# Kernel tuning notes

Hardware: AMD Instinct MI355X
Metric: run time of the kernel (lower is better)

Reference implementation:

```python
import jax, jax.numpy as jnp
import numpy as np
from jax import lax

TEMP = 20.0    # args.temp
ATT_WT = 0.5   # args.att_wt
EPS = 1e-12


def l2norm(x, axis):
    # torch F.normalize: x / max(||x||_2, eps)
    n = jnp.sqrt(jnp.sum(x * x, axis=axis, keepdims=True))
    return x / jnp.maximum(n, EPS)


def conv4d(x, w):
    """4D conv, padding=1, stride=1.
    x: [B,Cin,H1,W1,H2,W2], w: [Cout,Cin,3,3,3,3] -> [B,Cout,H1,W1,H2,W2].
    Decomposed as 9 fixed (di,dj) shifts over (H1,W1), each a 2D conv over (H2,W2).
    """
    B, Cin, H1, W1, H2, W2 = x.shape
    Cout = w.shape[0]
    xp = jnp.pad(x, ((0, 0), (0, 0), (1, 1), (1, 1), (0, 0), (0, 0)))
    out = jnp.zeros((B * H1 * W1, Cout, H2, W2), x.dtype)
    for di in range(3):
        for dj in range(3):
            xs = xp[:, :, di:di + H1, dj:dj + W1]                      # [B,Cin,H1,W1,H2,W2]
            xr = xs.transpose(0, 2, 3, 1, 4, 5).reshape(B * H1 * W1, Cin, H2, W2)
            out = out + lax.conv_general_dilated(
                xr, w[:, :, di, dj], (1, 1), 'SAME',
                dimension_numbers=('NCHW', 'OIHW', 'NCHW'))
    return out.reshape(B, H1, W1, Cout, H2, W2).transpose(0, 3, 1, 2, 4, 5)


def nc_stack(x, ws):
    for w in ws:
        x = jax.nn.relu(conv4d(x, w))
    return x


def neigh_consensus(corr, ws):
    # symmetric mode: conv(C) + perm(conv(perm(C)))
    ct = corr.transpose(0, 1, 4, 5, 2, 3)
    return nc_stack(corr, ws) + nc_stack(ct, ws).transpose(0, 1, 4, 5, 2, 3)


def setup_inputs() -> dict:
    key = jax.random.key(0)
    ks = jax.random.split(key, 7)
    L, B, C, h, w = 9, 2, 1024, 20, 20
    ch = 256
    return {
        'fq_feats': jax.random.normal(ks[0], (L, B, C, h, w), jnp.float32),
        'fs_feats': jax.random.normal(ks[1], (L, B, C, h, w), jnp.float32),
        'f_q': jax.random.normal(ks[2], (B, ch, h, w), jnp.float32),
        'f_s': jax.random.normal(ks[3], (B, ch, h, w), jnp.float32),
        'w1': jax.random.normal(ks[4], (10, 9, 3, 3, 3, 3), jnp.float32) * 0.1,
        'w2': jax.random.normal(ks[5], (10, 10, 3, 3, 3, 3), jnp.float32) * 0.1,
        'w3': jax.random.normal(ks[6], (1, 10, 3, 3, 3, 3), jnp.float32) * 0.1,
    }


def reference(fq_feats, fs_feats, f_q, f_s, w1, w2, w3):
    L, B, C, h, w = fq_feats.shape
    ch = f_q.shape[1]
    hw = h * w
    # per-level channel-wise L2 normalization -> cosine correlation volume
    fqn = l2norm(fq_feats, axis=2)
    fsn = l2norm(fs_feats, axis=2)
    # corr4d[b,l,i,j,k,m] = <fq[:, i,j], fs[:, k,m]>  -> [B, L, h, w, h, w]
    corr4d = jnp.einsum('lbcij,lbckm->blijkm', fqn, fsn)
    # neighbourhood-consensus matching net -> [B,1,h,w,h,w]
    c4 = neigh_consensus(corr4d, (w1, w2, w3))
    attn = jax.nn.softmax(c4.reshape(B, hw, hw) * TEMP, axis=-1)  # over support positions
    v = f_s.reshape(B, ch, hw)
    att_fq = jnp.einsum('bqs,bcs->bcq', attn, v).reshape(B, ch, h, w)
    fq = l2norm(f_q, axis=1) + l2norm(att_fq, axis=1) * ATT_WT
    return (fq, att_fq)
```

## Files before the change

### kernel.cpp

```cpp
#include <hip/hip_runtime.h>
#include <math.h>
#include <stddef.h>

#define L9   9
#define NB   2
#define CF   1024
#define HW   400
#define CH   256
#define TEMPF 20.0f
#define EPSF  1e-12f

typedef _Float16 half8 __attribute__((ext_vector_type(8)));
typedef float f32x4 __attribute__((ext_vector_type(4)));
typedef unsigned short ushort_t;

__global__ __launch_bounds__(256) void norm_partial2(const float* __restrict__ fq,
                                                     const float* __restrict__ fs,
                                                     float* __restrict__ partial2) {
    int chunk = blockIdx.x, lb = blockIdx.y, t = blockIdx.z;
    int tid = threadIdx.x;
    if (tid >= 200) return;
    int half = tid / 100, p4 = tid - half * 100;
    const float* src = (t == 0 ? fq : fs) + (size_t)lb * CF * HW + p4 * 4;
    int c0 = chunk * 64 + half;
    f32x4 acc = {};
    #pragma unroll 8
    for (int it = 0; it < 32; ++it) {
        const float4 v = *(const float4*)(src + (size_t)(c0 + it * 2) * HW);
        acc[0] = fmaf(v.x, v.x, acc[0]);
        acc[1] = fmaf(v.y, v.y, acc[1]);
        acc[2] = fmaf(v.z, v.z, acc[2]);
        acc[3] = fmaf(v.w, v.w, acc[3]);
    }
    float* dst = partial2 + ((size_t)((t * 18 + lb) * 32) + chunk * 2 + half) * HW + p4 * 4;
    *(f32x4*)dst = acc;
}

__global__ __launch_bounds__(256) void norm_finalize2(const float* __restrict__ partial2,
                                                      float* __restrict__ invn) {
    int idx = blockIdx.x * 256 + threadIdx.x;
    if (idx >= 2 * 18 * HW) return;
    int t_lb = idx / HW;
    int ij = idx - t_lb * HW;
    const float* p = partial2 + (size_t)t_lb * 32 * HW + ij;
    float ss = 0.f;
    #pragma unroll
    for (int c = 0; c < 32; ++c) ss += p[c * HW];
    invn[idx] = 1.0f / fmaxf(sqrtf(ss), EPSF);
}

__global__ __launch_bounds__(256) void transpose_f16(const float* __restrict__ fq,
                                                     const float* __restrict__ fs,
                                                     ushort_t* __restrict__ At,
                                                     ushort_t* __restrict__ Bt,
                                                     int lb_base) {
    __shared__ float tile[64][65];
    int z = blockIdx.z;
    int tsel = z / 9, li = z - tsel * 9;
    int lb = lb_base + li;
    const float* src = (tsel ? fs : fq) + (size_t)lb * CF * HW;
    ushort_t* dst = (tsel ? Bt : At) + (size_t)li * HW * CF;
    int c0 = blockIdx.x * 64, ij0 = blockIdx.y * 64;
    int tid = threadIdx.x;
    int cl = tid >> 6;
    int col = tid & 63;
    #pragma unroll
    for (int rr = 0; rr < 16; ++rr) {
        int c_local = rr * 4 + cl;
        int ij = ij0 + col;
        tile[c_local][col] = (ij < HW) ? src[(size_t)(c0 + c_local) * HW + ij] : 0.f;
    }
    __syncthreads();
    int cp = (tid & 31) * 2;
    int rowsel = tid >> 5;
    #pragma unroll
    for (int rr = 0; rr < 8; ++rr) {
        int ij_local = rr * 8 + rowsel;
        int ij = ij0 + ij_local;
        if (ij < HW) {
            union { _Float16 h; ushort_t u; } h0, h1;
            h0.h = (_Float16)tile[cp][ij_local];
            h1.h = (_Float16)tile[cp + 1][ij_local];
            ushort2 o; o.x = h0.u; o.y = h1.u;
            *(ushort2*)(dst + (size_t)ij * CF + c0 + cp) = o;
        }
    }
}

__global__ __launch_bounds__(256) void corr_gemm_mfma(const ushort_t* __restrict__ At,
                                                      const ushort_t* __restrict__ Bt,
                                                      const float* __restrict__ invn,
                                                      ushort_t* __restrict__ corr,
                                                      int lb_base) {
    __shared__ ushort_t As[64][72];
    __shared__ ushort_t Bs[64][72];
    int li = blockIdx.z, lb = lb_base + li;
    int l = lb >> 1, b = lb & 1;
    int i0 = blockIdx.y * 64, j0 = blockIdx.x * 64;
    int tid = threadIdx.x, lane = tid & 63, w = tid >> 6;
    int mw = (w >> 1) * 32, nw = (w & 1) * 32;
    f32x4 acc[2][2] = {};
    const ushort_t* Abase = At + (size_t)li * HW * CF;
    const ushort_t* Bbase = Bt + (size_t)li * HW * CF;

    for (int kt = 0; kt < 16; ++kt) {
        int c0 = kt * 64;
        __syncthreads();
        #pragma unroll
        for (int p = 0; p < 2; ++p) {
            int idx = tid + p * 256;
            int row = idx >> 3, c8 = idx & 7;
            uint4 va = make_uint4(0, 0, 0, 0), vb = make_uint4(0, 0, 0, 0);
            if (i0 + row < HW) va = *(const uint4*)(Abase + (size_t)(i0 + row) * CF + c0 + c8 * 8);
            if (j0 + row < HW) vb = *(const uint4*)(Bbase + (size_t)(j0 + row) * CF + c0 + c8 * 8);
            *(uint4*)&As[row][c8 * 8] = va;
            *(uint4*)&Bs[row][c8 * 8] = vb;
        }
        __syncthreads();
        #pragma unroll
        for (int ks = 0; ks < 2; ++ks) {
            int k0 = ks * 32 + (lane >> 4) * 8;
            half8 a0 = *(const half8*)&As[mw + (lane & 15)][k0];
            half8 a1 = *(const half8*)&As[mw + 16 + (lane & 15)][k0];
            half8 b0 = *(const half8*)&Bs[nw + (lane & 15)][k0];
            half8 b1 = *(const half8*)&Bs[nw + 16 + (lane & 15)][k0];
            acc[0][0] = __builtin_amdgcn_mfma_f32_16x16x32_f16(a0, b0, acc[0][0], 0, 0, 0);
            acc[0][1] = __builtin_amdgcn_mfma_f32_16x16x32_f16(a0, b1, acc[0][1], 0, 0, 0);
            acc[1][0] = __builtin_amdgcn_mfma_f32_16x16x32_f16(a1, b0, acc[1][0], 0, 0, 0);
            acc[1][1] = __builtin_amdgcn_mfma_f32_16x16x32_f16(a1, b1, acc[1][1], 0, 0, 0);
        }
    }
    int obase = (b * 9 + l) * HW;
    #pragma unroll
    for (int mi = 0; mi < 2; ++mi) {
        #pragma unroll
        for (int ni = 0; ni < 2; ++ni) {
            #pragma unroll
            for (int r = 0; r < 4; ++r) {
                int ij = i0 + mw + mi * 16 + (lane >> 4) * 4 + r;
                int km = j0 + nw + ni * 16 + (lane & 15);
                if (ij < HW && km < HW) {
                    union { _Float16 h; ushort_t u; } cv;
                    cv.h = (_Float16)(acc[mi][ni][r] * invn[lb * HW + ij] * invn[7200 + lb * HW + km]);
                    corr[(size_t)(obase + ij) * HW + km] = cv.u;
                }
            }
        }
    }
}

template <int CIN, int COUT, bool SWAP>
__global__ __launch_bounds__(256) void wprep7(const float* __restrict__ wt,
                                              ushort_t* __restrict__ wb) {
    constexpr int S = CIN * 9;
    constexpr int NCH = (S + 31) / 32;
    int idx = blockIdx.x * 256 + threadIdx.x;
    int total = NCH * 4608;
    if (idx >= total) return;
    int k = idx & 31, n = (idx >> 5) & 15, dd = (idx >> 9) % 9, ch = idx / 4608;
    int slot = ch * 32 + k;
    float v = 0.f;
    if (n < COUT && slot < S) {
        int ci = slot / 9, pl = slot - ci * 9;
        int di = pl / 3, dj = pl % 3, dk = dd / 3, dm = dd % 3;
        int widx = SWAP ? ((((n * CIN + ci) * 3 + dk) * 3 + dm) * 3 + di) * 3 + dj
                        : ((((n * CIN + ci) * 3 + di) * 3 + dj) * 3 + dk) * 3 + dm;
        v = wt[widx];
    }
    union { _Float16 h; ushort_t u; } cv; cv.h = (_Float16)v;
    wb[idx] = cv.u;
}

template <int CIN, int COUT, bool SWAP, int MODE>
__global__ __launch_bounds__(256) void wprep12(const float* __restrict__ wt,
                                               ushort_t* __restrict__ wb) {
    constexpr int S2 = CIN * 12;
    constexpr int NCH = (S2 + 31) / 32;
    int idx = blockIdx.x * 256 + threadIdx.x;
    int total = NCH * 4608;
    if (idx >= total) return;
    int k = idx & 31, n = (idx >> 5) & 15, dd = (idx >> 9) % 9, ch = idx / 4608;
    int slot = ch * 32 + k;
    float v = 0.f;
    if (slot < S2) {
        int ci = slot / 12, r = slot - ci * 12;
        int di = r >> 2, dj4 = r & 3;
        int dk = dd / 3, dm = dd % 3;
        int off = (MODE == 2) ? n : MODE;
        int e = dj4 - off;
        int nn = (MODE == 2) ? 0 : n;
        bool ok = (MODE == 2) ? (n < 2) : (n < COUT);
        if (ok && e >= 0 && e <= 2) {
            int widx = SWAP ? ((((nn * CIN + ci) * 3 + dk) * 3 + dm) * 3 + di) * 3 + e
                            : ((((nn * CIN + ci) * 3 + di) * 3 + e) * 3 + dk) * 3 + dm;
            v = wt[widx];
        }
    }
    union { _Float16 h; ushort_t u; } cv; cv.h = (_Float16)v;
    wb[idx] = cv.u;
}

template <int CIN, int COUT>
__global__ __launch_bounds__(256) void conv4d_l1(const ushort_t* __restrict__ in,
                                                 const ushort_t* __restrict__ wbA,
                                                 const ushort_t* __restrict__ wbB,
                                                 ushort_t* __restrict__ outA,
                                                 ushort_t* __restrict__ outB) {
    constexpr int S = CIN * 9;
    constexpr int NCH = (S + 31) / 32;
    __shared__ __align__(16) ushort_t Ah[484 * 40];
    const int b = blockIdx.y, ij = blockIdx.x;
    const int i = ij / 20, j = ij - (ij / 20) * 20;
    const int tid = threadIdx.x, wv = tid >> 6, lane = tid & 63;
    const int m16 = lane & 15, q4 = lane >> 4;

    for (int p = tid; p < 484 * 20; p += 256) ((uint*)Ah)[p] = 0;

    int baseh[7];
    #pragma unroll
    for (int s = 0; s < 7; ++s) {
        int t = wv + 4 * s;
        if (t < 25) {
            int km = t * 16 + m16;
            int kk = km / 20, mm = km - kk * 20;
            baseh[s] = (kk * 22 + mm) * 40 + q4 * 8;
        } else baseh[s] = 0;
    }
    f32x4 accA[7] = {};
    f32x4 accB[7] = {};

    const bool stager = tid < 200;
    const int km1 = 2 * tid;
    const int r1 = stager ? ((km1 / 20 + 1) * 22 + (km1 % 20) + 1) : 0;
    int hofs[9]; bool vld[9];
    #pragma unroll
    for (int pl = 0; pl < 9; ++pl) {
        int ii = i + pl / 3 - 1, jj = j + pl % 3 - 1;
        vld[pl] = (unsigned)ii < 20u && (unsigned)jj < 20u;
        hofs[pl] = (ii * 20 + jj) * HW + km1;
    }
    const ushort_t* in_b = in + (size_t)b * CIN * HW * HW;
    const int wbase = m16 * 32 + q4 * 8;

    uint pf[32];
    #pragma unroll
    for (int u = 0; u < 32; ++u) {
        int slot = u;
        if (slot < S) {
            int ci = slot / 9, pl = slot - ci * 9;
            pf[u] = (stager && vld[pl]) ? *(const uint*)(in_b + ci * (HW * HW) + hofs[pl]) : 0u;
        } else pf[u] = 0u;
    }
    __syncthreads();

    #pragma unroll
    for (int ch = 0; ch < NCH; ++ch) {
        if (stager) {
            #pragma unroll
            for (int g4 = 0; g4 < 8; ++g4) {
                uint lo0 = (pf[4 * g4] & 0xFFFFu) | (pf[4 * g4 + 1] << 16);
                uint lo1 = (pf[4 * g4 + 2] & 0xFFFFu) | (pf[4 * g4 + 3] << 16);
                uint hi0 = (pf[4 * g4] >> 16) | (pf[4 * g4 + 1] & 0xFFFF0000u);
                uint hi1 = (pf[4 * g4 + 2] >> 16) | (pf[4 * g4 + 3] & 0xFFFF0000u);
                uint2 wlo; wlo.x = lo0; wlo.y = lo1;
                uint2 whi; whi.x = hi0; whi.y = hi1;
                *(uint2*)&Ah[(size_t)r1 * 40 + 4 * g4] = wlo;
                *(uint2*)&Ah[(size_t)(r1 + 1) * 40 + 4 * g4] = whi;
            }
        }
        __syncthreads();
        if (ch + 1 < NCH) {
            #pragma unroll
            for (int u = 0; u < 32; ++u) {
                int slot = (ch + 1) * 32 + u;
                if (slot < S) {
                    int ci = slot / 9, pl = slot - ci * 9;
                    pf[u] = (stager && vld[pl]) ? *(const uint*)(in_b + ci * (HW * HW) + hofs[pl]) : 0u;
                } else pf[u] = 0u;
            }
        }
        #pragma unroll
        for (int dd = 0; dd < 9; ++dd) {
            half8 bfA = *(const half8*)(wbA + (ch * 9 + dd) * 512 + wbase);
            half8 bfB = *(const half8*)(wbB + (ch * 9 + dd) * 512 + wbase);
            const int doff = ((dd / 3) * 22 + (dd % 3)) * 40;
            #pragma unroll
            for (int s = 0; s < 7; ++s) {
                if (wv + 4 * s < 25) {
                    half8 af = *(const half8*)(Ah + baseh[s] + doff);
                    accA[s] = __builtin_amdgcn_mfma_f32_16x16x32_f16(af, bfA, accA[s], 0, 0, 0);
                    accB[s] = __builtin_amdgcn_mfma_f32_16x16x32_f16(af, bfB, accB[s], 0, 0, 0);
                }
            }
        }
        if (ch + 1 < NCH) __syncthreads();
    }

    const int co = m16;
    if (co < COUT) {
        #pragma unroll
        for (int s = 0; s < 7; ++s) {
            int t = wv + 4 * s;
            if (t < 25) {
                int km0 = t * 16 + q4 * 4;
                size_t o = ((size_t)(b * COUT + co) * HW + ij) * HW + km0;
                union { ushort_t us[4]; uint2 u2; } pk;
                #pragma unroll
                for (int r = 0; r < 4; ++r) {
                    union { _Float16 h; ushort_t u16; } cv;
                    cv.h = (_Float16)fmaxf(accA[s][r], 0.f);
                    pk.us[r] = cv.u16;
                }
                *(uint2*)(outA + o) = pk.u2;
                #pragma unroll
                for (int r = 0; r < 4; ++r) {
                    union { _Float16 h; ushort_t u16; } cv;
                    cv.h = (_Float16)fmaxf(accB[s][r], 0.f);
                    pk.us[r] = cv.u16;
                }
                *(uint2*)(outB + o) = pk.u2;
            }
        }
    }
}

template <int CIN, int COUT, bool MERGED, bool OUTF16>
__global__ __launch_bounds__(256) void conv4d_2ij(
        const ushort_t* __restrict__ inA, const ushort_t* __restrict__ inB,
        const ushort_t* __restrict__ wA1, const ushort_t* __restrict__ wA2,
        const ushort_t* __restrict__ wB1, const ushort_t* __restrict__ wB2,
        void* __restrict__ outA, void* __restrict__ outB) {
    constexpr int S2 = CIN * 12;
    constexpr int NCH = (S2 + 31) / 32;
    __shared__ __align__(16) ushort_t Ah[484 * 40];
    const int b = blockIdx.y, bx = blockIdx.x, z = blockIdx.z;
    const ushort_t* in = z ? inB : inA;
    const ushort_t* w1 = z ? wB1 : wA1;
    const ushort_t* w2 = z ? wB2 : wA2;
    void* outS = z ? outB : outA;
    const int i = bx / 10, jp = bx - (bx / 10) * 10;
    const int j0 = 2 * jp;
    const int ij0 = i * 20 + j0;
    const int tid = threadIdx.x, wv = tid >> 6, lane = tid & 63;
    const int m16 = lane & 15, q4 = lane >> 4;

    for (int p = tid; p < 484 * 20; p += 256) ((uint*)Ah)[p] = 0;

    int baseh[7];
    #pragma unroll
    for (int s = 0; s < 7; ++s) {
        int t = wv + 4 * s;
        if (t < 25) {
            int km = t * 16 + m16;
            int kk = km / 20, mm = km - kk * 20;
            baseh[s] = (kk * 22 + mm) * 40 + q4 * 8;
        } else baseh[s] = 0;
    }
    f32x4 acc1[7] = {};
    f32x4 acc2[7] = {};

    const bool stager = tid < 200;
    const int km1 = 2 * tid;
    const int r1 = stager ? ((km1 / 20 + 1) * 22 + (km1 % 20) + 1) : 0;
    int hofs[12]; bool vld[12];
    #pragma unroll
    for (int pl = 0; pl < 12; ++pl) {
        int di = pl >> 2, dj = pl & 3;
        int ii = i + di - 1, jj = j0 + dj - 1;
        vld[pl] = (unsigned)ii < 20u && (unsigned)jj < 20u;
        hofs[pl] = (ii * 20 + jj) * HW + km1;
    }
    const ushort_t* in_b = in + (size_t)b * CIN * HW * HW;
    const int wbase = m16 * 32 + q4 * 8;

    uint pf[32];
    #pragma unroll
    for (int u = 0; u < 32; ++u) {
        int slot = u;
        if (slot < S2) {
            int ci = slot / 12, pl = slot - ci * 12;
            pf[u] = (stager && vld[pl]) ? *(const uint*)(in_b + ci * (HW * HW) + hofs[pl]) : 0u;
        } else pf[u] = 0u;
    }
    __syncthreads();

    #pragma unroll
    for (int ch = 0; ch < NCH; ++ch) {
        if (stager) {
            #pragma unroll
            for (int g4 = 0; g4 < 8; ++g4) {
                uint lo0 = (pf[4 * g4] & 0xFFFFu) | (pf[4 * g4 + 1] << 16);
                uint lo1 = (pf[4 * g4 + 2] & 0xFFFFu) | (pf[4 * g4 + 3] << 16);
                uint hi0 = (pf[4 * g4] >> 16) | (pf[4 * g4 + 1] & 0xFFFF0000u);
                uint hi1 = (pf[4 * g4 + 2] >> 16) | (pf[4 * g4 + 3] & 0xFFFF0000u);
                uint2 wlo; wlo.x = lo0; wlo.y = lo1;
                uint2 whi; whi.x = hi0; whi.y = hi1;
                *(uint2*)&Ah[(size_t)r1 * 40 + 4 * g4] = wlo;
                *(uint2*)&Ah[(size_t)(r1 + 1) * 40 + 4 * g4] = whi;
            }
        }
        __syncthreads();
        if (ch + 1 < NCH) {
            #pragma unroll
            for (int u = 0; u < 32; ++u) {
                int slot = (ch + 1) * 32 + u;
                if (slot < S2) {
                    int ci = slot / 12, pl = slot - ci * 12;
                    pf[u] = (stager && vld[pl]) ? *(const uint*)(in_b + ci * (HW * HW) + hofs[pl]) : 0u;
                } else pf[u] = 0u;
            }
        }
        #pragma unroll
        for (int dd = 0; dd < 9; ++dd) {
            half8 bf1 = *(const half8*)(w1 + (ch * 9 + dd) * 512 + wbase);
            half8 bf2;
            if (!MERGED) bf2 = *(const half8*)(w2 + (ch * 9 + dd) * 512 + wbase);
            const int doff = ((dd / 3) * 22 + (dd % 3)) * 40;
            #pragma unroll
            for (int s = 0; s < 7; ++s) {
                if (wv + 4 * s < 25) {
                    half8 af = *(const half8*)(Ah + baseh[s] + doff);
                    acc1[s] = __builtin_amdgcn_mfma_f32_16x16x32_f16(af, bf1, acc1[s], 0, 0, 0);
                    if (!MERGED) acc2[s] = __builtin_amdgcn_mfma_f32_16x16x32_f16(af, bf2, acc2[s], 0, 0, 0);
                }
            }
        }
        if (ch + 1 < NCH) __syncthreads();
    }

    if (MERGED) {
        if (m16 < 2) {
            const int ij = ij0 + m16;
            #pragma unroll
            for (int s = 0; s < 7; ++s) {
                int t = wv + 4 * s;
                if (t < 25) {
                    int km0 = t * 16 + q4 * 4;
                    size_t o = ((size_t)b * HW + ij) * HW + km0;
                    f32x4 ov;
                    #pragma unroll
                    for (int r = 0; r < 4; ++r) ov[r] = fmaxf(acc1[s][r], 0.f);
                    *(f32x4*)((float*)outS + o) = ov;
                }
            }
        }
    } else {
        const int co = m16;
        if (co < COUT) {
            #pragma unroll
            for (int s = 0; s < 7; ++s) {
                int t = wv + 4 * s;
                if (t < 25) {
                    int km0 = t * 16 + q4 * 4;
                    size_t o = ((size_t)(b * COUT + co) * HW + ij0) * HW + km0;
                    if (OUTF16) {
                        union { ushort_t us[4]; uint2 u2; } pk;
                        #pragma unroll
                        for (int r = 0; r < 4; ++r) {
                            union { _Float16 h; ushort_t u16; } cv;
                            cv.h = (_Float16)fmaxf(acc1[s][r], 0.f);
                            pk.us[r] = cv.u16;
                        }
                        *(uint2*)((ushort_t*)outS + o) = pk.u2;
                        #pragma unroll
                        for (int r = 0; r < 4; ++r) {
                            union { _Float16 h; ushort_t u16; } cv;
                            cv.h = (_Float16)fmaxf(acc2[s][r], 0.f);
                            pk.us[r] = cv.u16;
                        }
                        *(uint2*)((ushort_t*)outS + o + HW) = pk.u2;
                    } else {
                        f32x4 ov;
                        #pragma unroll
                        for (int r = 0; r < 4; ++r) ov[r] = fmaxf(acc1[s][r], 0.f);
                        *(f32x4*)((float*)outS + o) = ov;
                        #pragma unroll
                        for (int r = 0; r < 4; ++r) ov[r] = fmaxf(acc2[s][r], 0.f);
                        *(f32x4*)((float*)outS + o + HW) = ov;
                    }
                }
            }
        }
    }
}

__global__ __launch_bounds__(256) void fs_prep(const float* __restrict__ f_s,
                                               ushort_t* __restrict__ fsh) {
    int idx = blockIdx.x * 256 + threadIdx.x;
    if (idx >= NB * CH * 416) return;
    int s = idx % 416, bc = idx / 416;
    float v = (s < HW) ? f_s[(size_t)bc * HW + s] : 0.f;
    union { _Float16 h; ushort_t u; } cv; cv.h = (_Float16)v;
    fsh[idx] = cv.u;
}

__global__ __launch_bounds__(256) void softmax_av_mfma2(const float* __restrict__ c4A,
                                                        const float* __restrict__ c4B,
                                                        const ushort_t* __restrict__ fsh,
                                                        float* __restrict__ att) {
    __shared__ ushort_t P[64 * 424];
    __shared__ float invl[64];
    const int b = blockIdx.z, qb = blockIdx.x * 64;
    const int tid = threadIdx.x, wv = tid >> 6, lane = tid & 63;
    const int m16 = lane & 15, q4 = lane >> 4;
    const int lane16 = lane & 15, rg4 = lane >> 4;

    #pragma unroll 1
    for (int rg = 0; rg < 4; ++rg) {
        const int ql = wv * 16 + rg * 4 + rg4;
        int q = qb + ql; if (q > HW - 1) q = HW - 1;
        const float* rowA = c4A + ((size_t)b * HW + q) * HW;
        const float* rowB = c4B + ((size_t)b * HW + q) * HW;
        float4 v4[7];
        #pragma unroll
        for (int k4 = 0; k4 < 6; ++k4) {
            float4 a4 = *(const float4*)(rowA + 64 * k4 + lane16 * 4);
            float4 b4 = *(const float4*)(rowB + 64 * k4 + lane16 * 4);
            v4[k4] = make_float4(a4.x + b4.x, a4.y + b4.y, a4.z + b4.z, a4.w + b4.w);
        }
        if (lane16 < 4) {
            float4 a4 = *(const float4*)(rowA + 384 + lane16 * 4);
            float4 b4 = *(const float4*)(rowB + 384 + lane16 * 4);
            v4[6] = make_float4(a4.x + b4.x, a4.y + b4.y, a4.z + b4.z, a4.w + b4.w);
        } else {
            v4[6] = make_float4(-1e30f, -1e30f, -1e30f, -1e30f);
        }
        float mx = -1e30f;
        #pragma unroll
        for (int k4 = 0; k4 < 7; ++k4)
            mx = fmaxf(mx, fmaxf(fmaxf(v4[k4].x, v4[k4].y), fmaxf(v4[k4].z, v4[k4].w)));
        #pragma unroll
        for (int off = 8; off; off >>= 1) mx = fmaxf(mx, __shfl_xor(mx, off, 16));
        float sum = 0.f;
        #pragma unroll
        for (int k4 = 0; k4 < 7; ++k4) {
            if (k4 == 6 && lane16 >= 4) break;
            float e0 = __expf(TEMPF * (v4[k4].x - mx));
            float e1 = __expf(TEMPF * (v4[k4].y - mx));
            float e2 = __expf(TEMPF * (v4[k4].z - mx));
            float e3 = __expf(TEMPF * (v4[k4].w - mx));
            sum += e0 + e1 + e2 + e3;
            union { ushort_t us[4]; uint2 u2; } pk;
            union { _Float16 h; ushort_t u16; } cv;
            cv.h = (_Float16)e0; pk.us[0] = cv.u16;
            cv.h = (_Float16)e1; pk.us[1] = cv.u16;
            cv.h = (_Float16)e2; pk.us[2] = cv.u16;
            cv.h = (_Float16)e3; pk.us[3] = cv.u16;
            *(uint2*)&P[(size_t)ql * 424 + 64 * k4 + lane16 * 4] = pk.u2;
        }
        if (lane16 >= 4 && lane16 < 10) {
            uint2 z2; z2.x = 0; z2.y = 0;
            *(uint2*)&P[(size_t)ql * 424 + 384 + lane16 * 4] = z2;
        }
        #pragma unroll
        for (int off = 8; off; off >>= 1) sum += __shfl_xor(sum, off, 16);
        if (lane16 == 0) invl[ql] = 1.0f / sum;
    }

    half8 afr[13];
    #pragma unroll
    for (int ks = 0; ks < 13; ++ks)
        afr[ks] = *(const half8*)&P[(size_t)(wv * 16 + m16) * 424 + ks * 32 + q4 * 8];
    const ushort_t* fb = fsh + (size_t)b * CH * 416;
    #pragma unroll
    for (int ntl = 0; ntl < 2; ++ntl) {
        const int nt = blockIdx.y * 2 + ntl;
        const int c = nt * 16 + m16;
        const ushort_t* fc = fb + (size_t)c * 416 + q4 * 8;
        f32x4 acc = {};
        #pragma unroll
        for (int ks = 0; ks < 13; ++ks) {
            half8 bf = *(const half8*)(fc + ks * 32);
            acc = __builtin_amdgcn_mfma_f32_16x16x32_f16(afr[ks], bf, acc, 0, 0, 0);
        }
        #pragma unroll
        for (int r = 0; r < 4; ++r) {
            int ql = wv * 16 + q4 * 4 + r;
            int q = qb + ql;
            if (q < HW)
                att[((size_t)b * CH + c) * HW + q] = acc[r] * invl[ql];
        }
    }
}

__global__ __launch_bounds__(256) void final_fq(const float* __restrict__ f_q,
                                                const float* __restrict__ att,
                                                float* __restrict__ out_fq) {
    __shared__ float red[256];
    int b = blockIdx.y, q = blockIdx.x;
    int tid = threadIdx.x;
    size_t idx = (size_t)(b * CH + tid) * HW + q;
    float f = f_q[idx];
    float a = att[idx];
    red[tid] = f * f;
    __syncthreads();
    for (int s = 128; s > 0; s >>= 1) {
        if (tid < s) red[tid] += red[tid + s];
        __syncthreads();
    }
    float invf = 1.0f / fmaxf(sqrtf(red[0]), EPSF);
    __syncthreads();
    red[tid] = a * a;
    __syncthreads();
    for (int s = 128; s > 0; s >>= 1) {
        if (tid < s) red[tid] += red[tid + s];
        __syncthreads();
    }
    float inva = 1.0f / fmaxf(sqrtf(red[0]), EPSF);
    out_fq[idx] = f * invf + 0.5f * a * inva;
}

extern "C" void kernel_launch(void* const* d_in, const int* in_sizes, int n_in,
                              void* d_out, int out_size, void* d_ws, size_t ws_size,
                              hipStream_t stream) {
    const float* fq_feats = (const float*)d_in[0];
    const float* fs_feats = (const float*)d_in[1];
    const float* f_q      = (const float*)d_in[2];
    const float* f_s      = (const float*)d_in[3];
    const float* w1       = (const float*)d_in[4];
    const float* w2       = (const float*)d_in[5];
    const float* w3       = (const float*)d_in[6];
    float* out = (float*)d_out;

    float* ws      = (float*)d_ws;
    float* wbuf    = ws;
    float* invn    = wbuf + 115200;
    float* corr    = invn + 14400;
    float* buf1    = corr + 2880000;
    float* buf2    = buf1 + 3200000;
    float* att     = out + 204800;

    float* partial2 = buf1;
    ushort_t* corr_h = (ushort_t*)corr;
    ushort_t* fsh    = (ushort_t*)(corr + 1440000);
    float* c4A = corr + 1600000;
    float* c4B = corr + 1920000;
    ushort_t* At = (ushort_t*)buf1;
    ushort_t* Bt = (ushort_t*)buf2;
    ushort_t* b1A = (ushort_t*)buf1;
    ushort_t* b1B = b1A + 3200000;
    ushort_t* b2A = (ushort_t*)buf2;
    ushort_t* b2B = b2A + 3200000;

    ushort_t* wb0    = (ushort_t*)wbuf;
    ushort_t* wbL1A  = wb0;
    ushort_t* wbL1B  = wb0 + 13824;
    ushort_t* wbL2A0 = wb0 + 27648;
    ushort_t* wbL2A1 = wb0 + 46080;
    ushort_t* wbL2B0 = wb0 + 64512;
    ushort_t* wbL2B1 = wb0 + 82944;
    ushort_t* wbL3Am = wb0 + 101376;
    ushort_t* wbL3Bm = wb0 + 119808;

    norm_partial2<<<dim3(16, 18, 2), 256, 0, stream>>>(fq_feats, fs_feats, partial2);
    norm_finalize2<<<(2 * 18 * HW + 255) / 256, 256, 0, stream>>>(partial2, invn);

    wprep7<9, 10, false><<<54, 256, 0, stream>>>(w1, wbL1A);
    wprep7<9, 10, true ><<<54, 256, 0, stream>>>(w1, wbL1B);
    wprep12<10, 10, false, 0><<<72, 256, 0, stream>>>(w2, wbL2A0);
    wprep12<10, 10, false, 1><<<72, 256, 0, stream>>>(w2, wbL2A1);
    wprep12<10, 10, true,  0><<<72, 256, 0, stream>>>(w2, wbL2B0);
    wprep12<10, 10, true,  1><<<72, 256, 0, stream>>>(w2, wbL2B1);
    wprep12<10, 1, false, 2><<<72, 256, 0, stream>>>(w3, wbL3Am);
    wprep12<10, 1, true,  2><<<72, 256, 0, stream>>>(w3, wbL3Bm);
    fs_prep<<<(NB * CH * 416 + 255) / 256, 256, 0, stream>>>(f_s, fsh);

    for (int half = 0; half < 2; ++half) {
        int base = half * 9;
        transpose_f16<<<dim3(16, 7, 18), 256, 0, stream>>>(fq_feats, fs_feats, At, Bt, base);
        corr_gemm_mfma<<<dim3(7, 7, 9), 256, 0, stream>>>(At, Bt, invn, corr_h, base);
    }

    conv4d_l1<9, 10><<<dim3(400, NB, 1), 256, 0, stream>>>(
        corr_h, wbL1A, wbL1B, b1A, b1B);
    conv4d_2ij<10, 10, false, true><<<dim3(200, NB, 2), 256, 0, stream>>>(
        b1A, b1B, wbL2A0, wbL2A1, wbL2B0, wbL2B1, b2A, b2B);
    conv4d_2ij<10, 1, true, false><<<dim3(200, NB, 2), 256, 0, stream>>>(
        b2A, b2B, wbL3Am, wbL3Am, wbL3Bm, wbL3Bm, c4A, c4B);

    softmax_av_mfma2<<<dim3(7, 8, NB), 256, 0, stream>>>(c4A, c4B, fsh, att);
    final_fq<<<dim3(400, NB), 256, 0, stream>>>(f_q, att, out);

    (void)in_sizes; (void)n_in; (void)out_size; (void)ws_size;
}
```

Before: 364.4 us.

## Merge prep kernels, fuse norm into transpose, restructure layer-2 conv and final reduction

Replaces the eight weight-prep launches, the f_s conversion and the ssbuf clear with one prep_all kernel. Drops the separate two-pass norm kernels by accumulating squared sums in transpose_f16 with atomics and taking the inverse square root in the GEMM epilogue. Layer 2 now runs the single-ij 9-tap conv kernel with one weight set per z, replacing the 2-ij 12-slot variant. final_fq switches its tree reduction to wavefront shuffles. This saves launches and a pass over the features, but adds atomics and redoes the sqrt/division per output element.

```diff
diff --git a/kernel.cpp b/kernel.cpp
--- a/kernel.cpp
+++ b/kernel.cpp
@@ -14,47 +14,69 @@
 typedef float f32x4 __attribute__((ext_vector_type(4)));
 typedef unsigned short ushort_t;
 
-__global__ __launch_bounds__(256) void norm_partial2(const float* __restrict__ fq,
-                                                     const float* __restrict__ fs,
-                                                     float* __restrict__ partial2) {
-    int chunk = blockIdx.x, lb = blockIdx.y, t = blockIdx.z;
-    int tid = threadIdx.x;
-    if (tid >= 200) return;
-    int half = tid / 100, p4 = tid - half * 100;
-    const float* src = (t == 0 ? fq : fs) + (size_t)lb * CF * HW + p4 * 4;
-    int c0 = chunk * 64 + half;
-    f32x4 acc = {};
-    #pragma unroll 8
-    for (int it = 0; it < 32; ++it) {
-        const float4 v = *(const float4*)(src + (size_t)(c0 + it * 2) * HW);
-        acc[0] = fmaf(v.x, v.x, acc[0]);
-        acc[1] = fmaf(v.y, v.y, acc[1]);
-        acc[2] = fmaf(v.z, v.z, acc[2]);
-        acc[3] = fmaf(v.w, v.w, acc[3]);
-    }
-    float* dst = partial2 + ((size_t)((t * 18 + lb) * 32) + chunk * 2 + half) * HW + p4 * 4;
-    *(f32x4*)dst = acc;
-}
-
-__global__ __launch_bounds__(256) void norm_finalize2(const float* __restrict__ partial2,
-                                                      float* __restrict__ invn) {
-    int idx = blockIdx.x * 256 + threadIdx.x;
-    if (idx >= 2 * 18 * HW) return;
-    int t_lb = idx / HW;
-    int ij = idx - t_lb * HW;
-    const float* p = partial2 + (size_t)t_lb * 32 * HW + ij;
-    float ss = 0.f;
-    #pragma unroll
-    for (int c = 0; c < 32; ++c) ss += p[c * HW];
-    invn[idx] = 1.0f / fmaxf(sqrtf(ss), EPSF);
+__global__ __launch_bounds__(256) void prep_all(const float* __restrict__ w1,
+                                                const float* __restrict__ w2,
+                                                const float* __restrict__ w3,
+                                                const float* __restrict__ f_s,
+                                                ushort_t* __restrict__ wb0,
+                                                ushort_t* __restrict__ fsh,
+                                                float* __restrict__ ssbuf) {
+    int gid = blockIdx.x * 256 + threadIdx.x;
+    if (gid < NB * CH * 416) {
+        int s = gid % 416, bc = gid / 416;
+        float v = (s < HW) ? f_s[(size_t)bc * HW + s] : 0.f;
+        union { _Float16 h; ushort_t u; } cv; cv.h = (_Float16)v;
+        fsh[gid] = cv.u;
+    }
+    if (gid < 14400) ssbuf[gid] = 0.f;
+    if (gid < 6 * 18432) {
+        int job = gid / 18432, idx = gid - job * 18432;
+        int k = idx & 31, n = (idx >> 5) & 15, dd = (idx >> 9) % 9, ch = idx / 4608;
+        int dk = dd / 3, dm = dd % 3;
+        float v = 0.f;
+        if (job < 4) {
+            if (idx < 13824) {
+                int CIN = (job < 2) ? 9 : 10;
+                const float* wt = (job < 2) ? w1 : w2;
+                bool swap = job & 1;
+                int slot = ch * 32 + k;
+                if (n < 10 && slot < CIN * 9) {
+                    int ci = slot / 9, pl = slot - ci * 9;
+                    int di = pl / 3, dj = pl % 3;
+                    int widx = swap ? ((((n * CIN + ci) * 3 + dk) * 3 + dm) * 3 + di) * 3 + dj
+                                    : ((((n * CIN + ci) * 3 + di) * 3 + dj) * 3 + dk) * 3 + dm;
+                    v = wt[widx];
+                }
+                union { _Float16 h; ushort_t u; } cv; cv.h = (_Float16)v;
+                wb0[job * 13824 + idx] = cv.u;
+            }
+        } else {
+            bool swap = (job == 5);
+            int slot = ch * 32 + k;
+            if (slot < 120) {
+                int ci = slot / 12, r = slot - ci * 12;
+                int di = r >> 2, dj4 = r & 3;
+                int e = dj4 - n;
+                if (n < 2 && e >= 0 && e <= 2) {
+                    int widx = swap ? (((ci * 3 + dk) * 3 + dm) * 3 + di) * 3 + e
+                                    : (((ci * 3 + di) * 3 + e) * 3 + dk) * 3 + dm;
+                    v = w3[widx];
+                }
+            }
+            union { _Float16 h; ushort_t u; } cv; cv.h = (_Float16)v;
+            wb0[55296 + (job - 4) * 18432 + idx] = cv.u;
+        }
+    }
 }
 
 __global__ __launch_bounds__(256) void transpose_f16(const float* __restrict__ fq,
                                                      const float* __restrict__ fs,
                                                      ushort_t* __restrict__ At,
                                                      ushort_t* __restrict__ Bt,
+                                                     float* __restrict__ ssbuf,
                                                      int lb_base) {
     __shared__ float tile[64][65];
+    __shared__ float red4[4][64];
     int z = blockIdx.z;
     int tsel = z / 9, li = z - tsel * 9;
     int lb = lb_base + li;
@@ -64,13 +86,24 @@
     int tid = threadIdx.x;
     int cl = tid >> 6;
     int col = tid & 63;
+    float ssp = 0.f;
     #pragma unroll
     for (int rr = 0; rr < 16; ++rr) {
         int c_local = rr * 4 + cl;
         int ij = ij0 + col;
-        tile[c_local][col] = (ij < HW) ? src[(size_t)(c0 + c_local) * HW + ij] : 0.f;
-    }
+        float v = (ij < HW) ? src[(size_t)(c0 + c_local) * HW + ij] : 0.f;
+        tile[c_local][col] = v;
+        ssp = fmaf(v, v, ssp);
+    }
+    red4[cl][col] = ssp;
     __syncthreads();
+    if (cl == 0) {
+        int ij = ij0 + col;
+        if (ij < HW) {
+            float s4 = red4[0][col] + red4[1][col] + red4[2][col] + red4[3][col];
+            atomicAdd(&ssbuf[(size_t)(tsel * 18 + lb) * HW + ij], s4);
+        }
+    }
     int cp = (tid & 31) * 2;
     int rowsel = tid >> 5;
     #pragma unroll
@@ -89,7 +122,7 @@
 
 __global__ __launch_bounds__(256) void corr_gemm_mfma(const ushort_t* __restrict__ At,
                                                       const ushort_t* __restrict__ Bt,
-                                                      const float* __restrict__ invn,
+                                                      const float* __restrict__ ssbuf,
                                                       ushort_t* __restrict__ corr,
                                                       int lb_base) {
     __shared__ ushort_t As[64][72];
@@ -132,16 +165,19 @@
     }
     int obase = (b * 9 + l) * HW;
     #pragma unroll
-    for (int mi = 0; mi < 2; ++mi) {
-        #pragma unroll
-        for (int ni = 0; ni < 2; ++ni) {
+    for (int ni = 0; ni < 2; ++ni) {
+        int km = j0 + nw + ni * 16 + (lane & 15);
+        if (km >= HW) continue;
+        float ib = 1.0f / fmaxf(sqrtf(ssbuf[(size_t)(18 + lb) * HW + km]), EPSF);
+        #pragma unroll
+        for (int mi = 0; mi < 2; ++mi) {
             #pragma unroll
             for (int r = 0; r < 4; ++r) {
                 int ij = i0 + mw + mi * 16 + (lane >> 4) * 4 + r;
-                int km = j0 + nw + ni * 16 + (lane & 15);
-                if (ij < HW && km < HW) {
+                if (ij < HW) {
+                    float ia = 1.0f / fmaxf(sqrtf(ssbuf[(size_t)lb * HW + ij]), EPSF);
                     union { _Float16 h; ushort_t u; } cv;
-                    cv.h = (_Float16)(acc[mi][ni][r] * invn[lb * HW + ij] * invn[7200 + lb * HW + km]);
+                    cv.h = (_Float16)(acc[mi][ni][r] * ia * ib);
                     corr[(size_t)(obase + ij) * HW + km] = cv.u;
                 }
             }
@@ -149,67 +185,21 @@
     }
 }
 
-template <int CIN, int COUT, bool SWAP>
-__global__ __launch_bounds__(256) void wprep7(const float* __restrict__ wt,
-                                              ushort_t* __restrict__ wb) {
-    constexpr int S = CIN * 9;
-    constexpr int NCH = (S + 31) / 32;
-    int idx = blockIdx.x * 256 + threadIdx.x;
-    int total = NCH * 4608;
-    if (idx >= total) return;
-    int k = idx & 31, n = (idx >> 5) & 15, dd = (idx >> 9) % 9, ch = idx / 4608;
-    int slot = ch * 32 + k;
-    float v = 0.f;
-    if (n < COUT && slot < S) {
-        int ci = slot / 9, pl = slot - ci * 9;
-        int di = pl / 3, dj = pl % 3, dk = dd / 3, dm = dd % 3;
-        int widx = SWAP ? ((((n * CIN + ci) * 3 + dk) * 3 + dm) * 3 + di) * 3 + dj
-                        : ((((n * CIN + ci) * 3 + di) * 3 + dj) * 3 + dk) * 3 + dm;
-        v = wt[widx];
-    }
-    union { _Float16 h; ushort_t u; } cv; cv.h = (_Float16)v;
-    wb[idx] = cv.u;
-}
-
-template <int CIN, int COUT, bool SWAP, int MODE>
-__global__ __launch_bounds__(256) void wprep12(const float* __restrict__ wt,
-                                               ushort_t* __restrict__ wb) {
-    constexpr int S2 = CIN * 12;
-    constexpr int NCH = (S2 + 31) / 32;
-    int idx = blockIdx.x * 256 + threadIdx.x;
-    int total = NCH * 4608;
-    if (idx >= total) return;
-    int k = idx & 31, n = (idx >> 5) & 15, dd = (idx >> 9) % 9, ch = idx / 4608;
-    int slot = ch * 32 + k;
-    float v = 0.f;
-    if (slot < S2) {
-        int ci = slot / 12, r = slot - ci * 12;
-        int di = r >> 2, dj4 = r & 3;
-        int dk = dd / 3, dm = dd % 3;
-        int off = (MODE == 2) ? n : MODE;
-        int e = dj4 - off;
-        int nn = (MODE == 2) ? 0 : n;
-        bool ok = (MODE == 2) ? (n < 2) : (n < COUT);
-        if (ok && e >= 0 && e <= 2) {
-            int widx = SWAP ? ((((nn * CIN + ci) * 3 + dk) * 3 + dm) * 3 + di) * 3 + e
-                            : ((((nn * CIN + ci) * 3 + di) * 3 + e) * 3 + dk) * 3 + dm;
-            v = wt[widx];
-        }
-    }
-    union { _Float16 h; ushort_t u; } cv; cv.h = (_Float16)v;
-    wb[idx] = cv.u;
-}
-
-template <int CIN, int COUT>
-__global__ __launch_bounds__(256) void conv4d_l1(const ushort_t* __restrict__ in,
+template <int CIN, int COUT, bool DUAL, bool OUTF16>
+__global__ __launch_bounds__(256) void conv4d_v8(const ushort_t* __restrict__ inA,
+                                                 const ushort_t* __restrict__ inB,
                                                  const ushort_t* __restrict__ wbA,
                                                  const ushort_t* __restrict__ wbB,
-                                                 ushort_t* __restrict__ outA,
-                                                 ushort_t* __restrict__ outB) {
+                                                 void* __restrict__ outA,
+                                                 void* __restrict__ outB) {
     constexpr int S = CIN * 9;
     constexpr int NCH = (S + 31) / 32;
     __shared__ __align__(16) ushort_t Ah[484 * 40];
     const int b = blockIdx.y, ij = blockIdx.x;
+    const int z = blockIdx.z;
+    const ushort_t* in = (DUAL || z == 0) ? inA : inB;
+    const ushort_t* wbS = (DUAL || z == 0) ? wbA : wbB;
+    void* outS = (DUAL || z == 0) ? outA : outB;
     const int i = ij / 20, j = ij - (ij / 20) * 20;
     const int tid = threadIdx.x, wv = tid >> 6, lane = tid & 63;
     const int m16 = lane & 15, q4 = lane >> 4;
@@ -281,15 +271,16 @@
         }
         #pragma unroll
         for (int dd = 0; dd < 9; ++dd) {
-            half8 bfA = *(const half8*)(wbA + (ch * 9 + dd) * 512 + wbase);
-            half8 bfB = *(const half8*)(wbB + (ch * 9 + dd) * 512 + wbase);
+            half8 bfA = *(const half8*)(wbS + (ch * 9 + dd) * 512 + wbase);
+            half8 bfB;
+            if (DUAL) bfB = *(const half8*)(wbB + (ch * 9 + dd) * 512 + wbase);
             const int doff = ((dd / 3) * 22 + (dd % 3)) * 40;
             #pragma unroll
             for (int s = 0; s < 7; ++s) {
                 if (wv + 4 * s < 25) {
                     half8 af = *(const half8*)(Ah + baseh[s] + doff);
                     accA[s] = __builtin_amdgcn_mfma_f32_16x16x32_f16(af, bfA, accA[s], 0, 0, 0);
-                    accB[s] = __builtin_amdgcn_mfma_f32_16x16x32_f16(af, bfB, accB[s], 0, 0, 0);
+                    if (DUAL) accB[s] = __builtin_amdgcn_mfma_f32_16x16x32_f16(af, bfB, accB[s], 0, 0, 0);
                 }
             }
         }
@@ -304,40 +295,47 @@
             if (t < 25) {
                 int km0 = t * 16 + q4 * 4;
                 size_t o = ((size_t)(b * COUT + co) * HW + ij) * HW + km0;
-                union { ushort_t us[4]; uint2 u2; } pk;
-                #pragma unroll
-                for (int r = 0; r < 4; ++r) {
-                    union { _Float16 h; ushort_t u16; } cv;
-                    cv.h = (_Float16)fmaxf(accA[s][r], 0.f);
-                    pk.us[r] = cv.u16;
+                if (OUTF16) {
+                    union { ushort_t us[4]; uint2 u2; } pk;
+                    #pragma unroll
+                    for (int r = 0; r < 4; ++r) {
+                        union { _Float16 h; ushort_t u16; } cv;
+                        cv.h = (_Float16)fmaxf(accA[s][r], 0.f);
+                        pk.us[r] = cv.u16;
+                    }
+                    *(uint2*)((ushort_t*)outS + o) = pk.u2;
+                    if (DUAL) {
+                        #pragma unroll
+                        for (int r = 0; r < 4; ++r) {
+                            union { _Float16 h; ushort_t u16; } cv;
+                            cv.h = (_Float16)fmaxf(accB[s][r], 0.f);
+                            pk.us[r] = cv.u16;
+                        }
+                        *(uint2*)((ushort_t*)outB + o) = pk.u2;
+                    }
+                } else {
+                    f32x4 ov;
+                    #pragma unroll
+                    for (int r = 0; r < 4; ++r) ov[r] = fmaxf(accA[s][r], 0.f);
+                    *(f32x4*)((float*)outS + o) = ov;
                 }
-                *(uint2*)(outA + o) = pk.u2;
-                #pragma unroll
-                for (int r = 0; r < 4; ++r) {
-                    union { _Float16 h; ushort_t u16; } cv;
-                    cv.h = (_Float16)fmaxf(accB[s][r], 0.f);
-                    pk.us[r] = cv.u16;
-                }
-                *(uint2*)(outB + o) = pk.u2;
-            }
-        }
-    }
-}
-
-template <int CIN, int COUT, bool MERGED, bool OUTF16>
-__global__ __launch_bounds__(256) void conv4d_2ij(
+            }
+        }
+    }
+}
+
+template <int CIN>
+__global__ __launch_bounds__(256) void conv4d_l3(
         const ushort_t* __restrict__ inA, const ushort_t* __restrict__ inB,
-        const ushort_t* __restrict__ wA1, const ushort_t* __restrict__ wA2,
-        const ushort_t* __restrict__ wB1, const ushort_t* __restrict__ wB2,
-        void* __restrict__ outA, void* __restrict__ outB) {
+        const ushort_t* __restrict__ wAm, const ushort_t* __restrict__ wBm,
+        float* __restrict__ outA, float* __restrict__ outB) {
     constexpr int S2 = CIN * 12;
     constexpr int NCH = (S2 + 31) / 32;
     __shared__ __align__(16) ushort_t Ah[484 * 40];
     const int b = blockIdx.y, bx = blockIdx.x, z = blockIdx.z;
     const ushort_t* in = z ? inB : inA;
-    const ushort_t* w1 = z ? wB1 : wA1;
-    const ushort_t* w2 = z ? wB2 : wA2;
-    void* outS = z ? outB : outA;
+    const ushort_t* w1 = z ? wBm : wAm;
+    float* outS = z ? outB : outA;
     const int i = bx / 10, jp = bx - (bx / 10) * 10;
     const int j0 = 2 * jp;
     const int ij0 = i * 20 + j0;
@@ -357,7 +355,6 @@
         } else baseh[s] = 0;
     }
     f32x4 acc1[7] = {};
-    f32x4 acc2[7] = {};
 
     const bool stager = tid < 200;
     const int km1 = 2 * tid;
@@ -413,85 +410,33 @@
         #pragma unroll
         for (int dd = 0; dd < 9; ++dd) {
             half8 bf1 = *(const half8*)(w1 + (ch * 9 + dd) * 512 + wbase);
-            half8 bf2;
-            if (!MERGED) bf2 = *(const half8*)(w2 + (ch * 9 + dd) * 512 + wbase);
             const int doff = ((dd / 3) * 22 + (dd % 3)) * 40;
             #pragma unroll
             for (int s = 0; s < 7; ++s) {
                 if (wv + 4 * s < 25) {
                     half8 af = *(const half8*)(Ah + baseh[s] + doff);
                     acc1[s] = __builtin_amdgcn_mfma_f32_16x16x32_f16(af, bf1, acc1[s], 0, 0, 0);
-                    if (!MERGED) acc2[s] = __builtin_amdgcn_mfma_f32_16x16x32_f16(af, bf2, acc2[s], 0, 0, 0);
                 }
             }
         }
         if (ch + 1 < NCH) __syncthreads();
     }
 
-    if (MERGED) {
-        if (m16 < 2) {
-            const int ij = ij0 + m16;
-            #pragma unroll
-            for (int s = 0; s < 7; ++s) {
-                int t = wv + 4 * s;
-                if (t < 25) {
-                    int km0 = t * 16 + q4 * 4;
-                    size_t o = ((size_t)b * HW + ij) * HW + km0;
-                    f32x4 ov;
-                    #pragma unroll
-                    for (int r = 0; r < 4; ++r) ov[r] = fmaxf(acc1[s][r], 0.f);
-                    *(f32x4*)((float*)outS + o) = ov;
-                }
-            }
-        }
-    } else {
-        const int co = m16;
-        if (co < COUT) {
-            #pragma unroll
-            for (int s = 0; s < 7; ++s) {
-                int t = wv + 4 * s;
-                if (t < 25) {
-                    int km0 = t * 16 + q4 * 4;
-                    size_t o = ((size_t)(b * COUT + co) * HW + ij0) * HW + km0;
-                    if (OUTF16) {
-                        union { ushort_t us[4]; uint2 u2; } pk;
-                        #pragma unroll
-                        for (int r = 0; r < 4; ++r) {
-                            union { _Float16 h; ushort_t u16; } cv;
-                            cv.h = (_Float16)fmaxf(acc1[s][r], 0.f);
-                            pk.us[r] = cv.u16;
-                        }
-                        *(uint2*)((ushort_t*)outS + o) = pk.u2;
-                        #pragma unroll
-                        for (int r = 0; r < 4; ++r) {
-                            union { _Float16 h; ushort_t u16; } cv;
-                            cv.h = (_Float16)fmaxf(acc2[s][r], 0.f);
-                            pk.us[r] = cv.u16;
-                        }
-                        *(uint2*)((ushort_t*)outS + o + HW) = pk.u2;
-                    } else {
-                        f32x4 ov;
-                        #pragma unroll
-                        for (int r = 0; r < 4; ++r) ov[r] = fmaxf(acc1[s][r], 0.f);
-                        *(f32x4*)((float*)outS + o) = ov;
-                        #pragma unroll
-                        for (int r = 0; r < 4; ++r) ov[r] = fmaxf(acc2[s][r], 0.f);
-                        *(f32x4*)((float*)outS + o + HW) = ov;
-                    }
-                }
-            }
-        }
-    }
-}
-
-__global__ __launch_bounds__(256) void fs_prep(const float* __restrict__ f_s,
-                                               ushort_t* __restrict__ fsh) {
-    int idx = blockIdx.x * 256 + threadIdx.x;
-    if (idx >= NB * CH * 416) return;
-    int s = idx % 416, bc = idx / 416;
-    float v = (s < HW) ? f_s[(size_t)bc * HW + s] : 0.f;
-    union { _Float16 h; ushort_t u; } cv; cv.h = (_Float16)v;
-    fsh[idx] = cv.u;
+    if (m16 < 2) {
+        const int ij = ij0 + m16;
+        #pragma unroll
+        for (int s = 0; s < 7; ++s) {
+            int t = wv + 4 * s;
+            if (t < 25) {
+                int km0 = t * 16 + q4 * 4;
+                size_t o = ((size_t)b * HW + ij) * HW + km0;
+                f32x4 ov;
+                #pragma unroll
+                for (int r = 0; r < 4; ++r) ov[r] = fmaxf(acc1[s][r], 0.f);
+                *(f32x4*)(outS + o) = ov;
+            }
+        }
+    }
 }
 
 __global__ __launch_bounds__(256) void softmax_av_mfma2(const float* __restrict__ c4A,
@@ -586,27 +531,24 @@
 __global__ __launch_bounds__(256) void final_fq(const float* __restrict__ f_q,
                                                 const float* __restrict__ att,
                                                 float* __restrict__ out_fq) {
-    __shared__ float red[256];
+    __shared__ float2 red[4];
     int b = blockIdx.y, q = blockIdx.x;
-    int tid = threadIdx.x;
+    int tid = threadIdx.x, wv = tid >> 6, lane = tid & 63;
     size_t idx = (size_t)(b * CH + tid) * HW + q;
     float f = f_q[idx];
     float a = att[idx];
-    red[tid] = f * f;
+    float vf = f * f, va = a * a;
+    #pragma unroll
+    for (int off = 32; off; off >>= 1) {
+        vf += __shfl_xor(vf, off);
+        va += __shfl_xor(va, off);
+    }
+    if (lane == 0) red[wv] = make_float2(vf, va);
     __syncthreads();
-    for (int s = 128; s > 0; s >>= 1) {
-        if (tid < s) red[tid] += red[tid + s];
-        __syncthreads();
-    }
-    float invf = 1.0f / fmaxf(sqrtf(red[0]), EPSF);
-    __syncthreads();
-    red[tid] = a * a;
-    __syncthreads();
-    for (int s = 128; s > 0; s >>= 1) {
-        if (tid < s) red[tid] += red[tid + s];
-        __syncthreads();
-    }
-    float inva = 1.0f / fmaxf(sqrtf(red[0]), EPSF);
+    float sf = red[0].x + red[1].x + red[2].x + red[3].x;
+    float sa = red[0].y + red[1].y + red[2].y + red[3].y;
+    float invf = 1.0f / fmaxf(sqrtf(sf), EPSF);
+    float inva = 1.0f / fmaxf(sqrtf(sa), EPSF);
     out_fq[idx] = f * invf + 0.5f * a * inva;
 }
 
@@ -624,13 +566,12 @@
 
     float* ws      = (float*)d_ws;
     float* wbuf    = ws;
-    float* invn    = wbuf + 115200;
-    float* corr    = invn + 14400;
+    float* ssbuf   = wbuf + 115200;
+    float* corr    = ssbuf + 14400;
     float* buf1    = corr + 2880000;
     float* buf2    = buf1 + 3200000;
     float* att     = out + 204800;
 
-    float* partial2 = buf1;
     ushort_t* corr_h = (ushort_t*)corr;
     ushort_t* fsh    = (ushort_t*)(corr + 1440000);
     float* c4A = corr + 1600000;
@@ -642,41 +583,28 @@
     ushort_t* b2A = (ushort_t*)buf2;
     ushort_t* b2B = b2A + 3200000;
 
-    ushort_t* wb0    = (ushort_t*)wbuf;
-    ushort_t* wbL1A  = wb0;
-    ushort_t* wbL1B  = wb0 + 13824;
-    ushort_t* wbL2A0 = wb0 + 27648;
-    ushort_t* wbL2A1 = wb0 + 46080;
-    ushort_t* wbL2B0 = wb0 + 64512;
-    ushort_t* wbL2B1 = wb0 + 82944;
-    ushort_t* wbL3Am = wb0 + 101376;
-    ushort_t* wbL3Bm = wb0 + 119808;
-
-    norm_partial2<<<dim3(16, 18, 2), 256, 0, stream>>>(fq_feats, fs_feats, partial2);
-    norm_finalize2<<<(2 * 18 * HW + 255) / 256, 256, 0, stream>>>(partial2, invn);
-
-    wprep7<9, 10, false><<<54, 256, 0, stream>>>(w1, wbL1A);
-    wprep7<9, 10, true ><<<54, 256, 0, stream>>>(w1, wbL1B);
-    wprep12<10, 10, false, 0><<<72, 256, 0, stream>>>(w2, wbL2A0);
-    wprep12<10, 10, false, 1><<<72, 256, 0, stream>>>(w2, wbL2A1);
-    wprep12<10, 10, true,  0><<<72, 256, 0, stream>>>(w2, wbL2B0);
-    wprep12<10, 10, true,  1><<<72, 256, 0, stream>>>(w2, wbL2B1);
-    wprep12<10, 1, false, 2><<<72, 256, 0, stream>>>(w3, wbL3Am);
-    wprep12<10, 1, true,  2><<<72, 256, 0, stream>>>(w3, wbL3Bm);
-    fs_prep<<<(NB * CH * 416 + 255) / 256, 256, 0, stream>>>(f_s, fsh);
+    ushort_t* wb0   = (ushort_t*)wbuf;
+    ushort_t* wbL1A = wb0;
+    ushort_t* wbL1B = wb0 + 13824;
+    ushort_t* wbL2A = wb0 + 27648;
+    ushort_t* wbL2B = wb0 + 41472;
+    ushort_t* wbL3Am = wb0 + 55296;
+    ushort_t* wbL3Bm = wb0 + 73728;
+
+    prep_all<<<832, 256, 0, stream>>>(w1, w2, w3, f_s, wb0, fsh, ssbuf);
 
     for (int half = 0; half < 2; ++half) {
         int base = half * 9;
-        transpose_f16<<<dim3(16, 7, 18), 256, 0, stream>>>(fq_feats, fs_feats, At, Bt, base);
-        corr_gemm_mfma<<<dim3(7, 7, 9), 256, 0, stream>>>(At, Bt, invn, corr_h, base);
-    }
-
-    conv4d_l1<9, 10><<<dim3(400, NB, 1), 256, 0, stream>>>(
-        corr_h, wbL1A, wbL1B, b1A, b1B);
-    conv4d_2ij<10, 10, false, true><<<dim3(200, NB, 2), 256, 0, stream>>>(
-        b1A, b1B, wbL2A0, wbL2A1, wbL2B0, wbL2B1, b2A, b2B);
-    conv4d_2ij<10, 1, true, false><<<dim3(200, NB, 2), 256, 0, stream>>>(
-        b2A, b2B, wbL3Am, wbL3Am, wbL3Bm, wbL3Bm, c4A, c4B);
+        transpose_f16<<<dim3(16, 7, 18), 256, 0, stream>>>(fq_feats, fs_feats, At, Bt, ssbuf, base);
+        corr_gemm_mfma<<<dim3(7, 7, 9), 256, 0, stream>>>(At, Bt, ssbuf, corr_h, base);
+    }
+
+    conv4d_v8<9, 10, true, true><<<dim3(400, NB, 1), 256, 0, stream>>>(
+        corr_h, corr_h, wbL1A, wbL1B, b1A, b1B);
+    conv4d_v8<10, 10, false, true><<<dim3(400, NB, 2), 256, 0, stream>>>(
+        b1A, b1B, wbL2A, wbL2B, b2A, b2B);
+    conv4d_l3<10><<<dim3(200, NB, 2), 256, 0, stream>>>(
+        b2A, b2B, wbL3Am, wbL3Bm, c4A, c4B);
 
     softmax_av_mfma2<<<dim3(7, 8, NB), 256, 0, stream>>>(c4A, c4B, fsh, att);
     final_fq<<<dim3(400, NB), 256, 0, stream>>>(f_q, att, out);
```

After: 344.7 us. 1.06x faster.
